# Optimization experiments

Hardware: AMD Instinct MI355X
Metric: run time of the kernel (lower is better)

Reference implementation:

```python
import jax, jax.numpy as jnp
import numpy as np

N_EMBED = 1024
EMBED_DIM = 256

def setup_inputs() -> dict:
    key = jax.random.key(0)
    k1, k2 = jax.random.split(key)
    hidden_states = jax.random.normal(k1, (64, 32, 32, EMBED_DIM), dtype=jnp.float32)
    emb_weights = jax.random.normal(k2, (N_EMBED, EMBED_DIM), dtype=jnp.float32)
    return {"hidden_states": hidden_states, "emb_weights": emb_weights}

def reference(hidden_states, emb_weights):
    # flatten (B,H,W,C) -> (N, C) with C == embed_dim
    z_flat = hidden_states.reshape((-1, EMBED_DIM))
    # squared distance: ||z||^2 + ||e||^2 - 2 z.e
    distance = (
        jnp.sum(z_flat ** 2, axis=1, keepdims=True)
        + jnp.sum(emb_weights ** 2, axis=1)
        - 2.0 * jnp.dot(z_flat, emb_weights.T)
    )  # (N, n_embed)
    min_encoding_indices = jnp.argmin(distance, axis=1)  # (N,)
    z_q = jnp.take(emb_weights, min_encoding_indices, axis=0).reshape(hidden_states.shape)
    min_encoding_indices = min_encoding_indices.reshape(hidden_states.shape[0], -1)
    return z_q, min_encoding_indices
```

## Files before the change

kernel.cpp:

```cpp
#include <hip/hip_runtime.h>

typedef _Float16 half8  __attribute__((ext_vector_type(8)));
typedef _Float16 half4  __attribute__((ext_vector_type(4)));
typedef float    float4v __attribute__((ext_vector_type(4)));
typedef float    float8v __attribute__((ext_vector_type(8)));

#define N_ROWS  65536
#define N_CODES 1024
#define DIM     256
#define BM      128
#define NBLKS   (N_ROWS / BM)

__global__ __launch_bounds__(64)
void vq_prep(const float* __restrict__ emb, float* __restrict__ e_norm,
             _Float16* __restrict__ e_frag) {
    const int c = blockIdx.x, lane = threadIdx.x;
    const int l15 = c & 15, nt = c >> 4;
    float4v v = ((const float4v*)(emb + (size_t)c * DIM))[lane];
    half4 h, l;
    float ss = 0.f;
    #pragma unroll
    for (int j = 0; j < 4; ++j) {
        float x = v[j];
        ss += x * x;
        _Float16 hh = (_Float16)x;
        h[j] = hh;
        l[j] = (_Float16)(x - (float)hh);
    }
    const int ks = lane >> 3, q = (lane >> 1) & 3, jb = (lane & 1) * 4;
    _Float16* p = e_frag + ((size_t)(nt * 8 + ks)) * 1024 + (q * 16 + l15) * 8 + jb;
    *(half4*)p = h;
    *(half4*)(p + 512) = l;
    #pragma unroll
    for (int m = 32; m >= 1; m >>= 1) ss += __shfl_xor(ss, m, 64);
    if (lane == 0) e_norm[c] = ss;
}

__global__ __launch_bounds__(512, 2)
void vq_main(const float* __restrict__ z,
             const _Float16* __restrict__ e_frag,
             const float* __restrict__ e_norm,
             const float* __restrict__ emb,
             float* __restrict__ zq,
             float* __restrict__ idxf,
             int fused_gather) {
    __shared__ _Float16 sA[64 * 2 * 512];
    __shared__ float    s_nrm[N_CODES];
    __shared__ float2   s_best[BM][17];
    __shared__ int      s_idx[BM];

    const int t = threadIdx.x;
    const int w = t >> 6, lane = t & 63, quad = lane >> 4, l15 = lane & 15;
    const int rowblk = blockIdx.x * BM;

    s_nrm[t] = e_norm[t];
    s_nrm[t + 512] = e_norm[t + 512];

    #pragma unroll
    for (int i = 0; i < 8; ++i) {
        const int mt = i, ks = w;
        const int row = mt * 16 + l15;
        const int col = ks * 32 + quad * 8;
        float8v v = *(const float8v*)(z + (size_t)(rowblk + row) * DIM + col);
        half8 h, lo;
        #pragma unroll
        for (int j = 0; j < 8; ++j) {
            float x = v[j];
            _Float16 hh = (_Float16)x;
            h[j] = hh;
            lo[j] = (_Float16)(x - (float)hh);
        }
        _Float16* p = sA + (size_t)((mt * 8 + ks) * 2) * 512 + lane * 8;
        *(half8*)p = h;
        *(half8*)(p + 512) = lo;
    }
    __syncthreads();

    #pragma unroll
    for (int pass = 0; pass < 2; ++pass) {
        const int ntbase = w * 8 + pass * 4;
        float4v acc[8][4] = {};

        for (int ks = 0; ks < 8; ++ks) {
            half8 bh[4], bl[4];
            #pragma unroll
            for (int nt = 0; nt < 4; ++nt) {
                const _Float16* bp = e_frag + ((size_t)((ntbase + nt) * 8 + ks)) * 1024 + lane * 8;
                bh[nt] = *(const half8*)bp;
                bl[nt] = *(const half8*)(bp + 512);
            }
            #pragma unroll
            for (int mt = 0; mt < 8; ++mt) {
                const _Float16* ap = sA + (size_t)((mt * 8 + ks) * 2) * 512 + lane * 8;
                half8 ah = *(const half8*)ap;
                half8 al = *(const half8*)(ap + 512);
                #pragma unroll
                for (int nt = 0; nt < 4; ++nt) {
                    acc[mt][nt] = __builtin_amdgcn_mfma_f32_16x16x32_f16(ah, bh[nt], acc[mt][nt], 0, 0, 0);
                    acc[mt][nt] = __builtin_amdgcn_mfma_f32_16x16x32_f16(ah, bl[nt], acc[mt][nt], 0, 0, 0);
                    acc[mt][nt] = __builtin_amdgcn_mfma_f32_16x16x32_f16(al, bh[nt], acc[mt][nt], 0, 0, 0);
                }
            }
        }

        float nrm[4]; int cg[4];
        #pragma unroll
        for (int nt = 0; nt < 4; ++nt) {
            cg[nt]  = (ntbase + nt) * 16 + l15;
            nrm[nt] = s_nrm[cg[nt]];
        }
        #pragma unroll
        for (int mt = 0; mt < 8; ++mt) {
            #pragma unroll
            for (int r = 0; r < 4; ++r) {
                float bs = 0.f; int bi = 0;
                #pragma unroll
                for (int nt = 0; nt < 4; ++nt) {
                    float s = nrm[nt] - 2.0f * acc[mt][nt][r];
                    if (nt == 0 || s < bs) { bs = s; bi = cg[nt]; }
                }
                #pragma unroll
                for (int m = 1; m < 16; m <<= 1) {
                    float s2 = __shfl_xor(bs, m, 64);
                    int   i2 = __shfl_xor(bi, m, 64);
                    if (s2 < bs || (s2 == bs && i2 < bi)) { bs = s2; bi = i2; }
                }
                if (l15 == 0) {
                    const int row = mt * 16 + quad * 4 + r;
                    float2 pr; pr.x = bs; pr.y = (float)bi;
                    s_best[row][w * 2 + pass] = pr;
                }
            }
        }
    }
    __syncthreads();

    if (t < BM) {
        float2 p0 = s_best[t][0];
        float bs = p0.x, bi = p0.y;
        #pragma unroll
        for (int s = 1; s < 16; ++s) {
            float2 pv = s_best[t][s];
            if (pv.x < bs || (pv.x == bs && pv.y < bi)) { bs = pv.x; bi = pv.y; }
        }
        s_idx[t] = (int)bi;
        idxf[rowblk + t] = bi;
    }

    if (!fused_gather) return;
    __syncthreads();

    const float4v* emb4 = (const float4v*)emb;
    float4v* zq4 = (float4v*)zq;
    const int rr = t >> 2, cb = t & 3;
    const int code = s_idx[rr];
    #pragma unroll
    for (int i = 0; i < 16; ++i) {
        const int chunk = cb + i * 4;
        zq4[(size_t)(rowblk + rr) * 64 + chunk] = emb4[(size_t)code * 64 + chunk];
    }
}

__global__ __launch_bounds__(256)
void vq_gather(const float* __restrict__ emb,
               const float* __restrict__ idxf,
               float* __restrict__ zq) {
    const int tid  = blockIdx.x * 256 + threadIdx.x;
    const int r    = tid >> 6;
    const int lane = tid & 63;
    const int idx  = (int)idxf[r];
    const float4* ep = (const float4*)(emb + (size_t)idx * DIM);
    ((float4*)(zq + (size_t)r * DIM))[lane] = ep[lane];
}

extern "C" void kernel_launch(void* const* d_in, const int* in_sizes, int n_in,
                              void* d_out, int out_size, void* d_ws, size_t ws_size,
                              hipStream_t stream) {
    const float* z   = (const float*)d_in[0];
    const float* emb = (const float*)d_in[1];

    float* zq   = (float*)d_out;
    float* idxf = zq + (size_t)N_ROWS * DIM;

    const size_t need = 4096 + (size_t)N_CODES * DIM * 2 * sizeof(_Float16);
    const int in_ws = (ws_size >= need);
    char* base = in_ws ? (char*)d_ws : (char*)d_out;
    float*    e_norm = (float*)base;
    _Float16* e_frag = (_Float16*)(base + 4096);

    vq_prep<<<N_CODES, 64, 0, stream>>>(emb, e_norm, e_frag);
    vq_main<<<NBLKS, 512, 0, stream>>>(z, e_frag, e_norm, emb, zq, idxf, in_ws);
    if (!in_ws)
        vq_gather<<<(N_ROWS * 64) / 256, 256, 0, stream>>>(emb, idxf, zq);
}
```

Baseline: 233.7 us.

## Stage codebook quarter in LDS, stream z from global, split codes across blocks

```diff
diff --git a/kernel.cpp b/kernel.cpp
--- a/kernel.cpp
+++ b/kernel.cpp
@@ -3,13 +3,10 @@
 typedef _Float16 half8  __attribute__((ext_vector_type(8)));
 typedef _Float16 half4  __attribute__((ext_vector_type(4)));
 typedef float    float4v __attribute__((ext_vector_type(4)));
-typedef float    float8v __attribute__((ext_vector_type(8)));
 
 #define N_ROWS  65536
 #define N_CODES 1024
 #define DIM     256
-#define BM      128
-#define NBLKS   (N_ROWS / BM)
 
 __global__ __launch_bounds__(64)
 void vq_prep(const float* __restrict__ emb, float* __restrict__ e_norm,
@@ -40,125 +37,121 @@
 void vq_main(const float* __restrict__ z,
              const _Float16* __restrict__ e_frag,
              const float* __restrict__ e_norm,
-             const float* __restrict__ emb,
-             float* __restrict__ zq,
-             float* __restrict__ idxf,
-             int fused_gather) {
-    __shared__ _Float16 sA[64 * 2 * 512];
-    __shared__ float    s_nrm[N_CODES];
-    __shared__ float2   s_best[BM][17];
-    __shared__ int      s_idx[BM];
+             float2* __restrict__ partial) {
+    __shared__ alignas(16) _Float16 sB[65536];
 
     const int t = threadIdx.x;
     const int w = t >> 6, lane = t & 63, quad = lane >> 4, l15 = lane & 15;
-    const int rowblk = blockIdx.x * BM;
+    const int bx = blockIdx.x;
+    const int cg = (bx >> 3) & 3;
+    const int rb = (bx & 7) | ((bx >> 5) << 3);
+    const int rowbase = rb * 512 + w * 64;
 
-    s_nrm[t] = e_norm[t];
-    s_nrm[t + 512] = e_norm[t + 512];
+    float bs[4][4];
+    int   bi[4][4];
+    #pragma unroll
+    for (int mt = 0; mt < 4; ++mt)
+        #pragma unroll
+        for (int r = 0; r < 4; ++r) { bs[mt][r] = 3.4e38f; bi[mt][r] = 0; }
 
-    #pragma unroll
-    for (int i = 0; i < 8; ++i) {
-        const int mt = i, ks = w;
-        const int row = mt * 16 + l15;
-        const int col = ks * 32 + quad * 8;
-        float8v v = *(const float8v*)(z + (size_t)(rowblk + row) * DIM + col);
-        half8 h, lo;
+    for (int p = 0; p < 2; ++p) {
+        if (p) __syncthreads();
+        {
+            const _Float16* gsrc = e_frag + (size_t)(16 * cg + 8 * p) * 8192;
+            #pragma unroll
+            for (int rr = 0; rr < 16; ++rr) {
+                const int off = rr * 4096 + t * 8;
+                *(half8*)(sB + off) = *(const half8*)(gsrc + off);
+            }
+        }
+        __syncthreads();
+
+        float nrm[8];
         #pragma unroll
-        for (int j = 0; j < 8; ++j) {
-            float x = v[j];
-            _Float16 hh = (_Float16)x;
-            h[j] = hh;
-            lo[j] = (_Float16)(x - (float)hh);
-        }
-        _Float16* p = sA + (size_t)((mt * 8 + ks) * 2) * 512 + lane * 8;
-        *(half8*)p = h;
-        *(half8*)(p + 512) = lo;
-    }
-    __syncthreads();
+        for (int ntl = 0; ntl < 8; ++ntl)
+            nrm[ntl] = e_norm[cg * 256 + p * 128 + ntl * 16 + l15];
 
-    #pragma unroll
-    for (int pass = 0; pass < 2; ++pass) {
-        const int ntbase = w * 8 + pass * 4;
-        float4v acc[8][4] = {};
+        float4v acc[4][8] = {};
 
         for (int ks = 0; ks < 8; ++ks) {
-            half8 bh[4], bl[4];
+            half8 ah[4], al[4];
             #pragma unroll
-            for (int nt = 0; nt < 4; ++nt) {
-                const _Float16* bp = e_frag + ((size_t)((ntbase + nt) * 8 + ks)) * 1024 + lane * 8;
-                bh[nt] = *(const half8*)bp;
-                bl[nt] = *(const half8*)(bp + 512);
+            for (int mt = 0; mt < 4; ++mt) {
+                const float* ap = z + (size_t)(rowbase + mt * 16 + l15) * DIM
+                                    + ks * 32 + quad * 8;
+                float4v a0 = *(const float4v*)ap;
+                float4v a1 = *(const float4v*)(ap + 4);
+                #pragma unroll
+                for (int j = 0; j < 4; ++j) {
+                    { float x = a0[j]; _Float16 hh = (_Float16)x;
+                      ah[mt][j] = hh; al[mt][j] = (_Float16)(x - (float)hh); }
+                    { float x = a1[j]; _Float16 hh = (_Float16)x;
+                      ah[mt][4 + j] = hh; al[mt][4 + j] = (_Float16)(x - (float)hh); }
+                }
             }
             #pragma unroll
-            for (int mt = 0; mt < 8; ++mt) {
-                const _Float16* ap = sA + (size_t)((mt * 8 + ks) * 2) * 512 + lane * 8;
-                half8 ah = *(const half8*)ap;
-                half8 al = *(const half8*)(ap + 512);
+            for (int ntl = 0; ntl < 8; ++ntl) {
+                const _Float16* bp = sB + (ntl * 8 + ks) * 1024 + lane * 8;
+                half8 bh = *(const half8*)bp;
+                half8 bl = *(const half8*)(bp + 512);
                 #pragma unroll
-                for (int nt = 0; nt < 4; ++nt) {
-                    acc[mt][nt] = __builtin_amdgcn_mfma_f32_16x16x32_f16(ah, bh[nt], acc[mt][nt], 0, 0, 0);
-                    acc[mt][nt] = __builtin_amdgcn_mfma_f32_16x16x32_f16(ah, bl[nt], acc[mt][nt], 0, 0, 0);
-                    acc[mt][nt] = __builtin_amdgcn_mfma_f32_16x16x32_f16(al, bh[nt], acc[mt][nt], 0, 0, 0);
+                for (int mt = 0; mt < 4; ++mt) {
+                    acc[mt][ntl] = __builtin_amdgcn_mfma_f32_16x16x32_f16(ah[mt], bh, acc[mt][ntl], 0, 0, 0);
+                    acc[mt][ntl] = __builtin_amdgcn_mfma_f32_16x16x32_f16(ah[mt], bl, acc[mt][ntl], 0, 0, 0);
+                    acc[mt][ntl] = __builtin_amdgcn_mfma_f32_16x16x32_f16(al[mt], bh, acc[mt][ntl], 0, 0, 0);
                 }
             }
         }
 
-        float nrm[4]; int cg[4];
         #pragma unroll
-        for (int nt = 0; nt < 4; ++nt) {
-            cg[nt]  = (ntbase + nt) * 16 + l15;
-            nrm[nt] = s_nrm[cg[nt]];
-        }
+        for (int mt = 0; mt < 4; ++mt)
+            #pragma unroll
+            for (int ntl = 0; ntl < 8; ++ntl) {
+                const int code = cg * 256 + p * 128 + ntl * 16 + l15;
+                #pragma unroll
+                for (int r = 0; r < 4; ++r) {
+                    float s = nrm[ntl] - 2.0f * acc[mt][ntl][r];
+                    if (s < bs[mt][r]) { bs[mt][r] = s; bi[mt][r] = code; }
+                }
+            }
+    }
+
+    #pragma unroll
+    for (int m = 1; m < 16; m <<= 1)
         #pragma unroll
-        for (int mt = 0; mt < 8; ++mt) {
+        for (int mt = 0; mt < 4; ++mt)
             #pragma unroll
             for (int r = 0; r < 4; ++r) {
-                float bs = 0.f; int bi = 0;
-                #pragma unroll
-                for (int nt = 0; nt < 4; ++nt) {
-                    float s = nrm[nt] - 2.0f * acc[mt][nt][r];
-                    if (nt == 0 || s < bs) { bs = s; bi = cg[nt]; }
-                }
-                #pragma unroll
-                for (int m = 1; m < 16; m <<= 1) {
-                    float s2 = __shfl_xor(bs, m, 64);
-                    int   i2 = __shfl_xor(bi, m, 64);
-                    if (s2 < bs || (s2 == bs && i2 < bi)) { bs = s2; bi = i2; }
-                }
-                if (l15 == 0) {
-                    const int row = mt * 16 + quad * 4 + r;
-                    float2 pr; pr.x = bs; pr.y = (float)bi;
-                    s_best[row][w * 2 + pass] = pr;
+                float s2 = __shfl_xor(bs[mt][r], m, 64);
+                int   i2 = __shfl_xor(bi[mt][r], m, 64);
+                if (s2 < bs[mt][r] || (s2 == bs[mt][r] && i2 < bi[mt][r])) {
+                    bs[mt][r] = s2; bi[mt][r] = i2;
                 }
             }
-        }
+
+    if (l15 == 0) {
+        #pragma unroll
+        for (int mt = 0; mt < 4; ++mt)
+            #pragma unroll
+            for (int r = 0; r < 4; ++r) {
+                const int row = rowbase + mt * 16 + quad * 4 + r;
+                float2 pr; pr.x = bs[mt][r]; pr.y = (float)bi[mt][r];
+                partial[(size_t)row * 4 + cg] = pr;
+            }
     }
-    __syncthreads();
+}
 
-    if (t < BM) {
-        float2 p0 = s_best[t][0];
-        float bs = p0.x, bi = p0.y;
-        #pragma unroll
-        for (int s = 1; s < 16; ++s) {
-            float2 pv = s_best[t][s];
-            if (pv.x < bs || (pv.x == bs && pv.y < bi)) { bs = pv.x; bi = pv.y; }
-        }
-        s_idx[t] = (int)bi;
-        idxf[rowblk + t] = bi;
+__global__ __launch_bounds__(256)
+void vq_reduce(const float2* __restrict__ partial, float* __restrict__ idxf) {
+    const int r = blockIdx.x * 256 + threadIdx.x;
+    const float2* p = partial + (size_t)r * 4;
+    float bsv = p[0].x, biv = p[0].y;
+    #pragma unroll
+    for (int s = 1; s < 4; ++s) {
+        float2 v = p[s];
+        if (v.x < bsv || (v.x == bsv && v.y < biv)) { bsv = v.x; biv = v.y; }
     }
-
-    if (!fused_gather) return;
-    __syncthreads();
-
-    const float4v* emb4 = (const float4v*)emb;
-    float4v* zq4 = (float4v*)zq;
-    const int rr = t >> 2, cb = t & 3;
-    const int code = s_idx[rr];
-    #pragma unroll
-    for (int i = 0; i < 16; ++i) {
-        const int chunk = cb + i * 4;
-        zq4[(size_t)(rowblk + rr) * 64 + chunk] = emb4[(size_t)code * 64 + chunk];
-    }
+    idxf[r] = biv;
 }
 
 __global__ __launch_bounds__(256)
@@ -182,14 +175,15 @@
     float* zq   = (float*)d_out;
     float* idxf = zq + (size_t)N_ROWS * DIM;
 
-    const size_t need = 4096 + (size_t)N_CODES * DIM * 2 * sizeof(_Float16);
-    const int in_ws = (ws_size >= need);
-    char* base = in_ws ? (char*)d_ws : (char*)d_out;
-    float*    e_norm = (float*)base;
-    _Float16* e_frag = (_Float16*)(base + 4096);
+    const size_t need = 4096 + (size_t)N_CODES * DIM * 2 * sizeof(_Float16)
+                      + (size_t)N_ROWS * 4 * sizeof(float2);
+    char* base = (ws_size >= need) ? (char*)d_ws : (char*)d_out;
+    float*    e_norm  = (float*)base;
+    _Float16* e_frag  = (_Float16*)(base + 4096);
+    float2*   partial = (float2*)(e_frag + (size_t)N_CODES * DIM * 2);
 
     vq_prep<<<N_CODES, 64, 0, stream>>>(emb, e_norm, e_frag);
-    vq_main<<<NBLKS, 512, 0, stream>>>(z, e_frag, e_norm, emb, zq, idxf, in_ws);
-    if (!in_ws)
-        vq_gather<<<(N_ROWS * 64) / 256, 256, 0, stream>>>(emb, idxf, zq);
+    vq_main<<<512, 512, 0, stream>>>(z, e_frag, e_norm, partial);
+    vq_reduce<<<N_ROWS / 256, 256, 0, stream>>>(partial, idxf);
+    vq_gather<<<(N_ROWS * 64) / 256, 256, 0, stream>>>(emb, idxf, zq);
 }
```

Result: no change. 238.4 us (+2.0%).
